# Performance work log

Measured on AMD Instinct MI355X. Metric: run time of the kernel, lower is better.

## Reference

```python
import jax, jax.numpy as jnp
import numpy as np

N_NODES = 50000
N_EDGES = 800000
C = 256
R = 4

def setup_inputs() -> dict:
    key = jax.random.key(0)
    ks = jax.random.split(key, 8)
    node_features = jax.random.normal(ks[0], (N_NODES, C), dtype=jnp.float32)
    edge_index = jax.random.randint(ks[1], (2, N_EDGES), 0, N_NODES, dtype=jnp.int64)
    edge_type = jax.random.randint(ks[2], (N_EDGES,), 0, R, dtype=jnp.int64)
    # RGCNConv params (glorot-ish scale)
    s = 1.0 / np.sqrt(C)
    rel_weight = jax.random.normal(ks[3], (R, C, C), dtype=jnp.float32) * s
    root_weight = jax.random.normal(ks[4], (C, C), dtype=jnp.float32) * s
    rgcn_bias = jax.random.normal(ks[5], (C,), dtype=jnp.float32) * 0.01
    att_weight = jax.random.normal(ks[6], (1, 2 * C), dtype=jnp.float32) * (1.0 / np.sqrt(2 * C))
    att_bias = jax.random.normal(ks[7], (1,), dtype=jnp.float32) * 0.01
    return {
        'node_features': node_features,
        'edge_index': edge_index,
        'edge_type': edge_type,
        'rel_weight': rel_weight,
        'root_weight': root_weight,
        'rgcn_bias': rgcn_bias,
        'att_weight': att_weight,
        'att_bias': att_bias,
    }


def _rgcn(node_features, edge_index, edge_type, rel_weight, root_weight, rgcn_bias):
    # PyG RGCNConv: per-relation mean aggregation of x_src @ W_r, plus root transform + bias.
    N = node_features.shape[0]
    src, dst = edge_index[0], edge_index[1]
    out = node_features @ root_weight + rgcn_bias  # [N, O]
    num_rel = rel_weight.shape[0]
    for r in range(num_rel):  # small fixed relation count
        trans = node_features @ rel_weight[r]          # [N, O] node-level transform
        mask = (edge_type == r)
        msg = jnp.where(mask[:, None], trans[src], 0.0)  # [E, O] masked gather
        ssum = jax.ops.segment_sum(msg, dst, num_segments=N)
        cnt = jax.ops.segment_sum(mask.astype(node_features.dtype), dst, num_segments=N)
        out = out + ssum / jnp.maximum(cnt, 1.0)[:, None]  # mean aggr; 0 where no edges
    return out


def reference(node_features, edge_index, edge_type, rel_weight, root_weight, rgcn_bias, att_weight, att_bias):
    u0 = _rgcn(node_features, edge_index, edge_type, rel_weight, root_weight, rgcn_bias)
    cat = jnp.concatenate([u0, node_features], axis=1)  # [N, 2O]
    a = jax.nn.sigmoid(cat @ att_weight.T + att_bias)   # [N, 1]
    h = jnp.tanh(u0) * a + node_features * (1.0 - a)
    return h
```

## Files before the change

kernel.cpp:

```cpp
#include <hip/hip_runtime.h>
#include <hip/hip_bf16.h>

#define C 256
#define NOUT 1280
#define BK 32

typedef __attribute__((ext_vector_type(8))) short bf16x8;
typedef __attribute__((ext_vector_type(4))) float f32x4;
typedef __attribute__((ext_vector_type(4))) unsigned short us4;

#define GLL16(g, l)                                                         \
  __builtin_amdgcn_global_load_lds(                                         \
      (const __attribute__((address_space(1))) void*)(g),                   \
      (__attribute__((address_space(3))) void*)(l), 16, 0, 0)

__device__ __forceinline__ float bf2f(unsigned short u) {
  return __uint_as_float(((unsigned int)u) << 16);
}
__device__ __forceinline__ unsigned short f2bf(float f) {
  unsigned int x = __float_as_uint(f);
  unsigned int lsb = (x >> 16) & 1u;
  x += 0x7fffu + lsb;
  return (unsigned short)(x >> 16);
}

__global__ void k_pre(const float* __restrict__ X, const float* __restrict__ rel,
                      const float* __restrict__ root, const float* __restrict__ attw,
                      unsigned short* __restrict__ Xbf, unsigned short* __restrict__ WT2,
                      float* __restrict__ ax2, int* __restrict__ cnt,
                      int N, int rowsPad) {
  int b = blockIdx.x, t = threadIdx.x;
  if (b < NOUT) {
    int m = b >> 8, c = b & 255;
    const float* W = (m == 0) ? root : (rel + (size_t)(m - 1) * C * C);
    WT2[(size_t)b * C + t] = f2bf(W[(size_t)t * C + c]);
  } else if (b < NOUT + (rowsPad >> 2)) {
    int row = (b - NOUT) * 4 + (t >> 6);
    int lane = t & 63;
    if (row < N) {
      float4 v = reinterpret_cast<const float4*>(X + (size_t)row * C)[lane];
      float4 w2 = reinterpret_cast<const float4*>(attw + C)[lane];
      us4 o;
      o.x = f2bf(v.x); o.y = f2bf(v.y); o.z = f2bf(v.z); o.w = f2bf(v.w);
      reinterpret_cast<us4*>(Xbf)[(size_t)row * 64 + lane] = o;
      float p = v.x * w2.x + v.y * w2.y + v.z * w2.z + v.w * w2.w;
#pragma unroll
      for (int m2 = 32; m2 >= 1; m2 >>= 1) p += __shfl_xor(p, m2);
      if (lane == 0) ax2[row] = p;
    } else if (row < rowsPad) {
      us4 z; z.x = 0; z.y = 0; z.z = 0; z.w = 0;
      reinterpret_cast<us4*>(Xbf)[(size_t)row * 64 + lane] = z;
      if (lane == 0) ax2[row] = 0.f;
    }
  } else {
    int i = (b - NOUT - (rowsPad >> 2)) * 256 + t;
    if (i < N) cnt[i] = 0;
  }
}

__global__ void k_hist(const int* __restrict__ edst, int* __restrict__ cnt, int E) {
  int e = blockIdx.x * blockDim.x + threadIdx.x;
  if (e < E) atomicAdd(cnt + edst[e], 1);
}

__global__ void k_scan1(const int* __restrict__ cnt, int* __restrict__ rp,
                        int* __restrict__ bsum, int n) {
  __shared__ int s[512];
  int t = threadIdx.x;
  int i = blockIdx.x * 512 + t;
  int v = (i < n) ? cnt[i] : 0;
  s[t] = v;
  __syncthreads();
  for (int off = 1; off < 512; off <<= 1) {
    int add = (t >= off) ? s[t - off] : 0;
    __syncthreads();
    s[t] += add;
    __syncthreads();
  }
  if (i < n) rp[i] = s[t] - v;
  if (t == 511) bsum[blockIdx.x] = s[511];
}

__global__ void k_scan2(const int* __restrict__ bsum, int* __restrict__ boff,
                        int* __restrict__ rp, int nb, int n) {
  if (threadIdx.x == 0) {
    int run = 0;
    for (int b = 0; b < nb; ++b) { boff[b] = run; run += bsum[b]; }
    rp[n] = run;
  }
}

__global__ void k_scan3(int* __restrict__ rp, const int* __restrict__ boff,
                        int* __restrict__ cursor, int n) {
  int i = blockIdx.x * 512 + threadIdx.x;
  if (i < n) {
    int v = rp[i] + boff[blockIdx.x];
    rp[i] = v;
    cursor[i] = v;
  }
}

__global__ void k_fill(const int* __restrict__ esrc, const int* __restrict__ edst,
                       const int* __restrict__ etype, int* __restrict__ cursor,
                       unsigned int* __restrict__ sorted, int E) {
  int e = blockIdx.x * blockDim.x + threadIdx.x;
  if (e >= E) return;
  int d = edst[e];
  int pos = atomicAdd(cursor + d, 1);
  sorted[pos] = (unsigned int)esrc[e] | ((unsigned int)etype[e] << 28);
}

__global__ __launch_bounds__(256) void k_gemm(
    const unsigned short* __restrict__ Xbf, const unsigned short* __restrict__ WT2,
    unsigned short* __restrict__ Y, int rowsPad) {
  __shared__ unsigned short lds_a[2][128 * BK];
  __shared__ unsigned short lds_b[2][128 * BK];
  int tid = threadIdx.x;
  int wave = tid >> 6, lane = tid & 63;

  int nwg = gridDim.x, orig = blockIdx.x;
  int q = nwg >> 3, r = nwg & 7;
  int xcd = orig & 7, lin = orig >> 3;
  int wgid = (xcd < r ? xcd * (q + 1) : r * (q + 1) + (xcd - r) * q) + lin;
  int mblk = wgid / 10, nblk = wgid - mblk * 10;
  int row0 = mblk * 128, col0 = nblk * 128;
  int wr = wave >> 1, wc = wave & 1, lcol = lane & 15;

  const unsigned short* aSrc[2];
  const unsigned short* bSrc[2];
  int ldsOfs[2];
#pragma unroll
  for (int c2 = 0; c2 < 2; ++c2) {
    int off = (wave * 2 + c2) * 1024 + lane * 16;
    int rr = off >> 6;
    int lg8 = (((off >> 4) & 3) ^ ((rr >> 1) & 3)) * 8;
    aSrc[c2] = Xbf + (size_t)(row0 + rr) * C + lg8;
    bSrc[c2] = WT2 + (size_t)(col0 + rr) * C + lg8;
    ldsOfs[c2] = (wave * 2 + c2) * 1024;
  }

  int aoff[4], boff[4];
  int kb = (lane >> 4) * 16;
#pragma unroll
  for (int i = 0; i < 4; ++i) {
    int ar = wr * 64 + i * 16 + lcol;
    aoff[i] = ar * 64 + (kb ^ (((ar >> 1) & 3) << 4));
    int bc = wc * 64 + i * 16 + lcol;
    boff[i] = bc * 64 + (kb ^ (((bc >> 1) & 3) << 4));
  }

  f32x4 acc[4][4];
#pragma unroll
  for (int i = 0; i < 4; ++i)
#pragma unroll
    for (int j = 0; j < 4; ++j) {
      f32x4 z; z[0] = 0.f; z[1] = 0.f; z[2] = 0.f; z[3] = 0.f;
      acc[i][j] = z;
    }

  auto stage = [&](int buf, int ks) {
    int kofs = ks * BK;
#pragma unroll
    for (int c2 = 0; c2 < 2; ++c2) {
      GLL16(aSrc[c2] + kofs, (char*)&lds_a[buf][0] + ldsOfs[c2]);
      GLL16(bSrc[c2] + kofs, (char*)&lds_b[buf][0] + ldsOfs[c2]);
    }
  };

  stage(0, 0);
  __syncthreads();

#pragma unroll 2
  for (int ks = 0; ks < 8; ++ks) {
    int cur = ks & 1;
    if (ks + 1 < 8) stage(cur ^ 1, ks + 1);
    bf16x8 af[4], bfr[4];
#pragma unroll
    for (int i = 0; i < 4; ++i) {
      af[i]  = *reinterpret_cast<const bf16x8*>((const char*)&lds_a[cur][0] + aoff[i]);
      bfr[i] = *reinterpret_cast<const bf16x8*>((const char*)&lds_b[cur][0] + boff[i]);
    }
#pragma unroll
    for (int mr = 0; mr < 4; ++mr)
#pragma unroll
      for (int nc = 0; nc < 4; ++nc)
        acc[mr][nc] = __builtin_amdgcn_mfma_f32_16x16x32_bf16(af[mr], bfr[nc], acc[mr][nc], 0, 0, 0);
    __syncthreads();
  }

  int lrow4 = (lane >> 4) * 4;
#pragma unroll
  for (int mr = 0; mr < 4; ++mr) {
#pragma unroll
    for (int reg = 0; reg < 4; ++reg) {
      int rowg = row0 + wr * 64 + mr * 16 + lrow4 + reg;
#pragma unroll
      for (int nc = 0; nc < 4; ++nc) {
        int colg = col0 + wc * 64 + nc * 16 + lcol;
        Y[(size_t)rowg * NOUT + colg] = f2bf(acc[mr][nc][reg]);
      }
    }
  }
}

#define ACC(u, v)                                                            \
  do {                                                                       \
    float f0 = bf2f((v).x), f1 = bf2f((v).y), f2 = bf2f((v).z), f3 = bf2f((v).w); \
    switch ((u) >> 28) {                                                     \
      case 0: a0.x += f0; a0.y += f1; a0.z += f2; a0.w += f3; ++c0; break;   \
      case 1: a1.x += f0; a1.y += f1; a1.z += f2; a1.w += f3; ++c1; break;   \
      case 2: a2.x += f0; a2.y += f1; a2.z += f2; a2.w += f3; ++c2; break;   \
      default: a3.x += f0; a3.y += f1; a3.z += f2; a3.w += f3; ++c3; break;  \
    }                                                                        \
  } while (0)

__global__ void k_gg(const unsigned short* __restrict__ Y,
                     const unsigned int* __restrict__ sorted,
                     const int* __restrict__ rp, const float* __restrict__ X,
                     const float* __restrict__ bias, const float* __restrict__ attw,
                     const float* __restrict__ abp, const float* __restrict__ ax2,
                     float* __restrict__ out, int N) {
  int wave = threadIdx.x >> 6, lane = threadIdx.x & 63;
  int dst = blockIdx.x * 4 + wave;
  if (dst >= N) return;
  const us4* Yv = reinterpret_cast<const us4*>(Y);

  float4 a0 = make_float4(0, 0, 0, 0), a1 = a0, a2 = a0, a3 = a0;
  int c0 = 0, c1 = 0, c2 = 0, c3 = 0;
  int s = rp[dst], e2 = rp[dst + 1];

#define YIDX(u) ((size_t)((u) & 0x0FFFFFFFu) * 320 + (((u) >> 28) + 1) * 64 + lane)
  int e = s;
  for (; e + 8 <= e2; e += 8) {
    unsigned int u0 = sorted[e],     u1 = sorted[e + 1], u2 = sorted[e + 2], u3 = sorted[e + 3];
    unsigned int u4 = sorted[e + 4], u5 = sorted[e + 5], u6 = sorted[e + 6], u7 = sorted[e + 7];
    us4 v0 = Yv[YIDX(u0)], v1 = Yv[YIDX(u1)], v2 = Yv[YIDX(u2)], v3 = Yv[YIDX(u3)];
    us4 v4 = Yv[YIDX(u4)], v5 = Yv[YIDX(u5)], v6 = Yv[YIDX(u6)], v7 = Yv[YIDX(u7)];
    ACC(u0, v0); ACC(u1, v1); ACC(u2, v2); ACC(u3, v3);
    ACC(u4, v4); ACC(u5, v5); ACC(u6, v6); ACC(u7, v7);
  }
  for (; e + 4 <= e2; e += 4) {
    unsigned int u0 = sorted[e], u1 = sorted[e + 1], u2 = sorted[e + 2], u3 = sorted[e + 3];
    us4 v0 = Yv[YIDX(u0)], v1 = Yv[YIDX(u1)], v2 = Yv[YIDX(u2)], v3 = Yv[YIDX(u3)];
    ACC(u0, v0); ACC(u1, v1); ACC(u2, v2); ACC(u3, v3);
  }
  for (; e < e2; ++e) {
    unsigned int u = sorted[e];
    us4 v = Yv[YIDX(u)];
    ACC(u, v);
  }
#undef YIDX

  float s0 = 1.0f / (float)max(c0, 1);
  float s1 = 1.0f / (float)max(c1, 1);
  float s2 = 1.0f / (float)max(c2, 1);
  float s3 = 1.0f / (float)max(c3, 1);
  us4 rt = Yv[(size_t)dst * 320 + lane];
  float4 bi = reinterpret_cast<const float4*>(bias)[lane];
  float4 w1 = reinterpret_cast<const float4*>(attw)[lane];
  float4 u0;
  u0.x = a0.x * s0 + a1.x * s1 + a2.x * s2 + a3.x * s3 + bf2f(rt.x) + bi.x;
  u0.y = a0.y * s0 + a1.y * s1 + a2.y * s2 + a3.y * s3 + bf2f(rt.y) + bi.y;
  u0.z = a0.z * s0 + a1.z * s1 + a2.z * s2 + a3.z * s3 + bf2f(rt.z) + bi.z;
  u0.w = a0.w * s0 + a1.w * s1 + a2.w * s2 + a3.w * s3 + bf2f(rt.w) + bi.w;

  float p = u0.x * w1.x + u0.y * w1.y + u0.z * w1.z + u0.w * w1.w;
#pragma unroll
  for (int m2 = 32; m2 >= 1; m2 >>= 1) p += __shfl_xor(p, m2);
  float a = 1.0f / (1.0f + expf(-(p + ax2[dst] + abp[0])));
  float b = 1.0f - a;
  float4 x4 = reinterpret_cast<const float4*>(X + (size_t)dst * C)[lane];
  float4 h;
  h.x = tanhf(u0.x) * a + x4.x * b;
  h.y = tanhf(u0.y) * a + x4.y * b;
  h.z = tanhf(u0.z) * a + x4.z * b;
  h.w = tanhf(u0.w) * a + x4.w * b;
  reinterpret_cast<float4*>(out + (size_t)dst * C)[lane] = h;
}

extern "C" void kernel_launch(void* const* d_in, const int* in_sizes, int n_in,
                              void* d_out, int out_size, void* d_ws, size_t ws_size,
                              hipStream_t stream) {
  const float* X     = (const float*)d_in[0];
  const int*   eidx  = (const int*)d_in[1];
  const int*   etype = (const int*)d_in[2];
  const float* rel   = (const float*)d_in[3];
  const float* root  = (const float*)d_in[4];
  const float* bias  = (const float*)d_in[5];
  const float* attw  = (const float*)d_in[6];
  const float* ab    = (const float*)d_in[7];
  float* out = (float*)d_out;

  int N = in_sizes[0] / C;
  int E = in_sizes[2];
  int rowsPad = ((N + 127) / 128) * 128;
  const int* esrc = eidx;
  const int* edst = eidx + E;

  char* w = (char*)d_ws;
  size_t off = 0;
  auto alloc = [&](size_t bytes) -> void* {
    void* p = w + off;
    off += (bytes + 255) & ~(size_t)255;
    return p;
  };
  unsigned short* Y    = (unsigned short*)alloc((size_t)rowsPad * NOUT * 2);
  unsigned short* Xbf  = (unsigned short*)alloc((size_t)rowsPad * C * 2);
  unsigned short* WT2  = (unsigned short*)alloc((size_t)NOUT * C * 2);
  float* ax2  = (float*)alloc((size_t)rowsPad * 4);
  int* cnt    = (int*)alloc((size_t)N * 4);
  int* rp     = (int*)alloc((size_t)(N + 1) * 4);
  int* cursor = (int*)alloc((size_t)N * 4);
  int* bsum   = (int*)alloc(1024);
  int* boffb  = (int*)alloc(1024);
  unsigned int* sorted = (unsigned int*)alloc((size_t)E * 4);

  int preBlocks = NOUT + (rowsPad >> 2) + (N + 255) / 256;
  k_pre<<<preBlocks, 256, 0, stream>>>(X, rel, root, attw, Xbf, WT2, ax2, cnt, N, rowsPad);
  k_gemm<<<(rowsPad / 128) * 10, 256, 0, stream>>>(Xbf, WT2, Y, rowsPad);
  k_hist<<<(E + 255) / 256, 256, 0, stream>>>(edst, cnt, E);
  int NB = (N + 511) / 512;
  k_scan1<<<NB, 512, 0, stream>>>(cnt, rp, bsum, N);
  k_scan2<<<1, 64, 0, stream>>>(bsum, boffb, rp, NB, N);
  k_scan3<<<NB, 512, 0, stream>>>(rp, boffb, cursor, N);
  k_fill<<<(E + 255) / 256, 256, 0, stream>>>(esrc, edst, etype, cursor, sorted, E);
  k_gg<<<(N + 3) / 4, 256, 0, stream>>>(Y, sorted, rp, X, bias, attw, ab, ax2, out, N);
}
```

Before: 256.9 us.

## Coalesce GEMM epilogue via LDS, tile weight transpose, single-kernel scan

Stages the GEMM output tile in swizzled LDS so each thread writes 16-byte contiguous chunks of Y instead of scattered 2-byte stores. Replaces the per-column weight transpose with 64x64 LDS-tiled transposes, and merges the three-kernel scan into one 1024-thread block that does a serial chunk scan. Also fully unrolls the k-loop and moves the CSR build before the GEMM. The single-block scan serializes work on one CU, and the epilogue adds an extra LDS round trip and barrier.

New measurement: 348.1 us. 35.5% more time.

```diff
diff --git a/kernel.cpp b/kernel.cpp
--- a/kernel.cpp
+++ b/kernel.cpp
@@ -29,13 +29,34 @@
                       unsigned short* __restrict__ Xbf, unsigned short* __restrict__ WT2,
                       float* __restrict__ ax2, int* __restrict__ cnt,
                       int N, int rowsPad) {
+  __shared__ float tw[64][65];
   int b = blockIdx.x, t = threadIdx.x;
-  if (b < NOUT) {
-    int m = b >> 8, c = b & 255;
+  if (b < 80) {
+    int m = b >> 4, tile = b & 15;
+    int ti = tile >> 2, tj = tile & 3;
     const float* W = (m == 0) ? root : (rel + (size_t)(m - 1) * C * C);
-    WT2[(size_t)b * C + t] = f2bf(W[(size_t)t * C + c]);
-  } else if (b < NOUT + (rowsPad >> 2)) {
-    int row = (b - NOUT) * 4 + (t >> 6);
+    int row = t >> 2, cj = (t & 3) * 16;
+    const float* src = W + (size_t)(ti * 64 + row) * C + tj * 64 + cj;
+#pragma unroll
+    for (int j = 0; j < 4; ++j) {
+      float4 v = reinterpret_cast<const float4*>(src)[j];
+      tw[row][cj + j * 4 + 0] = v.x;
+      tw[row][cj + j * 4 + 1] = v.y;
+      tw[row][cj + j * 4 + 2] = v.z;
+      tw[row][cj + j * 4 + 3] = v.w;
+    }
+    __syncthreads();
+    int c = t >> 2, k0 = (t & 3) * 16;
+    int n = m * 256 + tj * 64 + c;
+    unsigned short o[16];
+#pragma unroll
+    for (int k = 0; k < 16; ++k) o[k] = f2bf(tw[k0 + k][c]);
+#pragma unroll
+    for (int j = 0; j < 4; ++j)
+      *reinterpret_cast<us4*>(WT2 + (size_t)n * C + ti * 64 + k0 + j * 4) =
+          *reinterpret_cast<us4*>(&o[j * 4]);
+  } else if (b < 80 + (rowsPad >> 2)) {
+    int row = (b - 80) * 4 + (t >> 6);
     int lane = t & 63;
     if (row < N) {
       float4 v = reinterpret_cast<const float4*>(X + (size_t)row * C)[lane];
@@ -53,7 +74,7 @@
       if (lane == 0) ax2[row] = 0.f;
     }
   } else {
-    int i = (b - NOUT - (rowsPad >> 2)) * 256 + t;
+    int i = (b - 80 - (rowsPad >> 2)) * 256 + t;
     if (i < N) cnt[i] = 0;
   }
 }
@@ -63,41 +84,31 @@
   if (e < E) atomicAdd(cnt + edst[e], 1);
 }
 
-__global__ void k_scan1(const int* __restrict__ cnt, int* __restrict__ rp,
-                        int* __restrict__ bsum, int n) {
-  __shared__ int s[512];
+__global__ __launch_bounds__(1024) void k_scan(const int* __restrict__ cnt,
+                                               int* __restrict__ rp,
+                                               int* __restrict__ cursor, int n) {
+  __shared__ int s[1024];
   int t = threadIdx.x;
-  int i = blockIdx.x * 512 + t;
-  int v = (i < n) ? cnt[i] : 0;
-  s[t] = v;
+  int chunk = (n + 1023) >> 10;
+  int lo = t * chunk, hi = min(lo + chunk, n);
+  int sum = 0;
+  for (int i = lo; i < hi; ++i) sum += cnt[i];
+  s[t] = sum;
   __syncthreads();
-  for (int off = 1; off < 512; off <<= 1) {
+  for (int off = 1; off < 1024; off <<= 1) {
     int add = (t >= off) ? s[t - off] : 0;
     __syncthreads();
     s[t] += add;
     __syncthreads();
   }
-  if (i < n) rp[i] = s[t] - v;
-  if (t == 511) bsum[blockIdx.x] = s[511];
-}
-
-__global__ void k_scan2(const int* __restrict__ bsum, int* __restrict__ boff,
-                        int* __restrict__ rp, int nb, int n) {
-  if (threadIdx.x == 0) {
-    int run = 0;
-    for (int b = 0; b < nb; ++b) { boff[b] = run; run += bsum[b]; }
-    rp[n] = run;
-  }
-}
-
-__global__ void k_scan3(int* __restrict__ rp, const int* __restrict__ boff,
-                        int* __restrict__ cursor, int n) {
-  int i = blockIdx.x * 512 + threadIdx.x;
-  if (i < n) {
-    int v = rp[i] + boff[blockIdx.x];
-    rp[i] = v;
-    cursor[i] = v;
-  }
+  int run = s[t] - sum;
+  for (int i = lo; i < hi; ++i) {
+    int v = cnt[i];
+    rp[i] = run;
+    cursor[i] = run;
+    run += v;
+  }
+  if (t == 1023) rp[n] = s[1023];
 }
 
 __global__ void k_fill(const int* __restrict__ esrc, const int* __restrict__ edst,
@@ -113,8 +124,9 @@
 __global__ __launch_bounds__(256) void k_gemm(
     const unsigned short* __restrict__ Xbf, const unsigned short* __restrict__ WT2,
     unsigned short* __restrict__ Y, int rowsPad) {
-  __shared__ unsigned short lds_a[2][128 * BK];
-  __shared__ unsigned short lds_b[2][128 * BK];
+  __shared__ unsigned short smem[16384];
+  unsigned short* ldsA = smem;
+  unsigned short* ldsB = smem + 8192;
   int tid = threadIdx.x;
   int wave = tid >> 6, lane = tid & 63;
 
@@ -162,23 +174,23 @@
     int kofs = ks * BK;
 #pragma unroll
     for (int c2 = 0; c2 < 2; ++c2) {
-      GLL16(aSrc[c2] + kofs, (char*)&lds_a[buf][0] + ldsOfs[c2]);
-      GLL16(bSrc[c2] + kofs, (char*)&lds_b[buf][0] + ldsOfs[c2]);
+      GLL16(aSrc[c2] + kofs, (char*)(ldsA + buf * 4096) + ldsOfs[c2]);
+      GLL16(bSrc[c2] + kofs, (char*)(ldsB + buf * 4096) + ldsOfs[c2]);
     }
   };
 
   stage(0, 0);
   __syncthreads();
 
-#pragma unroll 2
+#pragma unroll
   for (int ks = 0; ks < 8; ++ks) {
     int cur = ks & 1;
     if (ks + 1 < 8) stage(cur ^ 1, ks + 1);
     bf16x8 af[4], bfr[4];
 #pragma unroll
     for (int i = 0; i < 4; ++i) {
-      af[i]  = *reinterpret_cast<const bf16x8*>((const char*)&lds_a[cur][0] + aoff[i]);
-      bfr[i] = *reinterpret_cast<const bf16x8*>((const char*)&lds_b[cur][0] + boff[i]);
+      af[i]  = *reinterpret_cast<const bf16x8*>((const char*)(ldsA + cur * 4096) + aoff[i]);
+      bfr[i] = *reinterpret_cast<const bf16x8*>((const char*)(ldsB + cur * 4096) + boff[i]);
     }
 #pragma unroll
     for (int mr = 0; mr < 4; ++mr)
@@ -190,16 +202,24 @@
 
   int lrow4 = (lane >> 4) * 4;
 #pragma unroll
-  for (int mr = 0; mr < 4; ++mr) {
-#pragma unroll
-    for (int reg = 0; reg < 4; ++reg) {
-      int rowg = row0 + wr * 64 + mr * 16 + lrow4 + reg;
-#pragma unroll
-      for (int nc = 0; nc < 4; ++nc) {
-        int colg = col0 + wc * 64 + nc * 16 + lcol;
-        Y[(size_t)rowg * NOUT + colg] = f2bf(acc[mr][nc][reg]);
+  for (int mr = 0; mr < 4; ++mr)
+#pragma unroll
+    for (int nc = 0; nc < 4; ++nc)
+#pragma unroll
+      for (int reg = 0; reg < 4; ++reg) {
+        int rr = wr * 64 + mr * 16 + lrow4 + reg;
+        int cc = wc * 64 + nc * 16 + lcol;
+        smem[rr * 128 + ((((cc >> 3) + rr) & 15) << 3) + (cc & 7)] =
+            f2bf(acc[mr][nc][reg]);
       }
-    }
+  __syncthreads();
+#pragma unroll
+  for (int rnd = 0; rnd < 8; ++rnd) {
+    int rr = rnd * 16 + (tid >> 4);
+    int g = tid & 15;
+    int p = (g + rr) & 15;
+    bf16x8 v = *reinterpret_cast<const bf16x8*>(smem + rr * 128 + p * 8);
+    *reinterpret_cast<bf16x8*>(Y + (size_t)(row0 + rr) * NOUT + col0 + g * 8) = v;
   }
 }
 
@@ -311,18 +331,13 @@
   int* cnt    = (int*)alloc((size_t)N * 4);
   int* rp     = (int*)alloc((size_t)(N + 1) * 4);
   int* cursor = (int*)alloc((size_t)N * 4);
-  int* bsum   = (int*)alloc(1024);
-  int* boffb  = (int*)alloc(1024);
   unsigned int* sorted = (unsigned int*)alloc((size_t)E * 4);
 
-  int preBlocks = NOUT + (rowsPad >> 2) + (N + 255) / 256;
+  int preBlocks = 80 + (rowsPad >> 2) + (N + 255) / 256;
   k_pre<<<preBlocks, 256, 0, stream>>>(X, rel, root, attw, Xbf, WT2, ax2, cnt, N, rowsPad);
+  k_hist<<<(E + 255) / 256, 256, 0, stream>>>(edst, cnt, E);
+  k_scan<<<1, 1024, 0, stream>>>(cnt, rp, cursor, N);
+  k_fill<<<(E + 255) / 256, 256, 0, stream>>>(esrc, edst, etype, cursor, sorted, E);
   k_gemm<<<(rowsPad / 128) * 10, 256, 0, stream>>>(Xbf, WT2, Y, rowsPad);
-  k_hist<<<(E + 255) / 256, 256, 0, stream>>>(edst, cnt, E);
-  int NB = (N + 511) / 512;
-  k_scan1<<<NB, 512, 0, stream>>>(cnt, rp, bsum, N);
-  k_scan2<<<1, 64, 0, stream>>>(bsum, boffb, rp, NB, N);
-  k_scan3<<<NB, 512, 0, stream>>>(rp, boffb, cursor, N);
-  k_fill<<<(E + 255) / 256, 256, 0, stream>>>(esrc, edst, etype, cursor, sorted, E);
   k_gg<<<(N + 3) / 4, 256, 0, stream>>>(Y, sorted, rp, X, bias, attw, ab, ax2, out, N);
 }
```
